# Kernel optimization log

Hardware: AMD Instinct MI355X
Metric: run time of the kernel (lower is better)

The kernel has to match this reference:

```python
import jax, jax.numpy as jnp
import numpy as np
from jax import lax

D_MODEL, D_STATE, D_CONV, EXPAND = 64, 16, 4, 2
D_INNER = EXPAND * D_MODEL          # 128
DT_RANK = (D_MODEL + 15) // 16      # 4 = ceil(d_model/16), mamba_ssm 'auto'
B, L, N_IDX = 512, 256, 2048


def setup_inputs() -> dict:
    key = jax.random.key(0)
    ks = jax.random.split(key, 14)
    g = lambda k, shape, s: jax.random.normal(k, shape, jnp.float32) * s
    return {
        "reads": jax.random.normal(ks[0], (B, L, 4), jnp.float32),
        "sequenced_reads_indices": jax.random.randint(ks[1], (N_IDX,), 0, B),
        "exp_w": g(ks[2], (4, D_MODEL), 0.5),
        "exp_b": jnp.zeros((D_MODEL,), jnp.float32),
        "in_proj_w": g(ks[3], (D_MODEL, 2 * D_INNER), 0.1),
        "conv_w": g(ks[4], (D_INNER, 1, D_CONV), 0.3),
        "conv_b": jnp.zeros((D_INNER,), jnp.float32),
        "x_proj_w": g(ks[5], (D_INNER, DT_RANK + 2 * D_STATE), 0.1),
        "dt_w": g(ks[6], (DT_RANK, D_INNER), 0.3),
        "dt_b": jnp.full((D_INNER,), -4.6, jnp.float32),  # softplus(-4.6) ~ 0.01, mamba dt init scale
        "A_log": jnp.log(jnp.broadcast_to(jnp.arange(1, D_STATE + 1, dtype=jnp.float32), (D_INNER, D_STATE))),
        "D_skip": jnp.ones((D_INNER,), jnp.float32),
        "out_proj_w": g(ks[7], (D_INNER, D_MODEL), 0.1),
        "q_w": g(ks[8], (2 * D_MODEL, D_MODEL), 0.1),
        "q_b": jnp.zeros((D_MODEL,), jnp.float32),
        "k_w": g(ks[9], (2 * D_MODEL, D_MODEL), 0.1),
        "k_b": jnp.zeros((D_MODEL,), jnp.float32),
    }


def _mamba(x, in_proj_w, conv_w, conv_b, x_proj_w, dt_w, dt_b, A_log, D_skip, out_proj_w):
    # x: [b, l, d_model]
    xm, z = jnp.split(x @ in_proj_w, 2, axis=-1)  # each [b, l, d_inner]
    # causal depthwise conv over the sequence axis (pad left by d_conv-1, truncate to l)
    xc = lax.conv_general_dilated(
        xm.transpose(0, 2, 1), conv_w, (1,), [(D_CONV - 1, 0)],
        dimension_numbers=("NCH", "OIH", "NCH"), feature_group_count=D_INNER)
    xc = jax.nn.silu(xc + conv_b[None, :, None]).transpose(0, 2, 1)  # [b, l, d_inner]
    dt, Bm, Cm = jnp.split(xc @ x_proj_w, [DT_RANK, DT_RANK + D_STATE], axis=-1)
    delta = jax.nn.softplus(dt @ dt_w + dt_b)  # [b, l, d_inner]
    A = -jnp.exp(A_log)                        # [d_inner, d_state]

    def step(h, inp):
        d_t, B_t, C_t, u_t = inp  # [b,di], [b,ds], [b,ds], [b,di]
        h = jnp.exp(d_t[:, :, None] * A) * h + (d_t * u_t)[:, :, None] * B_t[:, None, :]
        return h, jnp.einsum("bdn,bn->bd", h, C_t)

    h0 = jnp.zeros((x.shape[0], D_INNER, D_STATE), x.dtype)
    xs = (delta.transpose(1, 0, 2), Bm.transpose(1, 0, 2),
          Cm.transpose(1, 0, 2), xc.transpose(1, 0, 2))
    _, ys = lax.scan(jax.checkpoint(step), h0, xs)  # ys: [l, b, d_inner]
    y = ys.transpose(1, 0, 2) + xc * D_skip
    return (y * jax.nn.silu(z)) @ out_proj_w  # [b, l, d_model]


def reference(reads, sequenced_reads_indices, exp_w, exp_b, in_proj_w, conv_w, conv_b,
              x_proj_w, dt_w, dt_b, A_log, D_skip, out_proj_w, q_w, q_b, k_w, k_b):
    x = reads @ exp_w + exp_b  # [b, l, d_model]
    enc = _mamba(x, in_proj_w, conv_w, conv_b, x_proj_w, dt_w, dt_b, A_log, D_skip, out_proj_w)
    mean_pooled = enc.mean(axis=1)        # [b, d_model]
    last_pooled = enc[:, -1, :]           # [b, d_model] (max pool computed in torch but unused)
    pooled = jnp.concatenate([mean_pooled, last_pooled], axis=-1)  # [b, 2*d_model]
    seq = pooled[sequenced_reads_indices]  # [n, 2*d_model]
    queries = seq @ q_w + q_b
    keys = pooled @ k_w + k_b
    return jnp.einsum("nd,md->nm", queries, keys)  # [n, b]
```

## Files before the change

kernel.cpp:

```cpp
#include <hip/hip_runtime.h>
#include <math.h>

#define L_SEQ 256
#define TILE 16
#define NSEG 16

typedef __attribute__((ext_vector_type(2))) float f32x2;
typedef __attribute__((ext_vector_type(4))) float f32x4;
typedef __attribute__((ext_vector_type(8))) _Float16 f16x8;
typedef __attribute__((ext_vector_type(4))) _Float16 f16x4;
typedef __attribute__((ext_vector_type(2))) _Float16 f16x2;

__device__ __forceinline__ f32x2 fma2(f32x2 a, f32x2 b, f32x2 c) {
    return __builtin_elementwise_fma(a, b, c);
}
__device__ __forceinline__ f32x2 splat2(float x) { f32x2 v = {x, x}; return v; }
__device__ __forceinline__ float rcp_f(float x) {
#if __has_builtin(__builtin_amdgcn_rcpf)
    return __builtin_amdgcn_rcpf(x);
#else
    return 1.f / x;
#endif
}
__device__ __forceinline__ float silu_f(float x) { return x * rcp_f(1.f + __expf(-x)); }

__global__ __launch_bounds__(256)
void k_prep(const float* __restrict__ exp_w, const float* __restrict__ exp_b,
            const float* __restrict__ in_proj_w, const float* __restrict__ x_proj_w,
            const float* __restrict__ dt_w,
            const float* __restrict__ conv_w, const float* __restrict__ conv_b,
            const float* __restrict__ A_log,
            _Float16* __restrict__ WT, _Float16* __restrict__ W2,
            float* __restrict__ bias2, int* __restrict__ sflag)
{
    const int t = threadIdx.x, blk = blockIdx.x;
    if (blk < 5) {
        const int base = blk * 4096;
        for (int i = base + t; i < base + 4096; i += 256) {
            const int row = i >> 7, k = i & 127;
            float v;
            if (row < 128) {
                v = x_proj_w[k * 36 + 0] * dt_w[row]
                  + x_proj_w[k * 36 + 1] * dt_w[128 + row]
                  + x_proj_w[k * 36 + 2] * dt_w[256 + row]
                  + x_proj_w[k * 36 + 3] * dt_w[384 + row];
            } else {
                v = x_proj_w[k * 36 + 4 + (row - 128)];
            }
            WT[i] = (_Float16)v;
        }
    } else if (blk == 5) {
        const int d = t & 127;
        const int col = (t < 128) ? d : (128 + d);
        float w0 = 0, w1 = 0, w2 = 0, w3 = 0, bb = 0;
        for (int k = 0; k < 64; ++k) {
            float w = in_proj_w[k * 256 + col];
            w0 = fmaf(exp_w[k], w, w0);
            w1 = fmaf(exp_w[64 + k], w, w1);
            w2 = fmaf(exp_w[128 + k], w, w2);
            w3 = fmaf(exp_w[192 + k], w, w3);
            bb = fmaf(exp_b[k], w, bb);
        }
        const float wx[4] = {w0, w1, w2, w3};
        if (t < 128) {
            for (int j = 0; j < 32; ++j) {
                float v = 0.f;
                if (j < 16)      v = conv_w[d * 4 + (j >> 2)] * wx[j & 3];
                else if (j < 20) v = conv_w[d * 4 + (j - 16)] * bb;
                W2[d * 32 + j] = (_Float16)v;
            }
            bias2[d] = conv_b[d];
        } else {
            for (int j = 0; j < 32; ++j) {
                float v = 0.f;
                if (j >= 12 && j < 16) v = wx[j - 12];
                else if (j == 19)      v = bb;
                W2[(128 + d) * 32 + j] = (_Float16)v;
            }
        }
    } else {
        __shared__ int ok;
        if (t == 0) ok = 1;
        __syncthreads();
        bool good = true;
        for (int i = t; i < 2048; i += 256) {
            float a = -__expf(A_log[i]);
            good = good && (fabsf(a + (float)((i & 15) + 1)) < 1e-3f);
        }
        if (!good) atomicAnd(&ok, 0);
        __syncthreads();
        if (t == 0) sflag[0] = ok;
    }
}

__global__ __launch_bounds__(256, 8)
void mamba_seg(const float* __restrict__ reads,
               const _Float16* __restrict__ WT, const _Float16* __restrict__ W2,
               const float* __restrict__ bias2, const float* __restrict__ dt_b,
               const float* __restrict__ A_log, const float* __restrict__ D_skip,
               const int* __restrict__ sflag,
               f16x2* __restrict__ Qg, f16x2* __restrict__ Pg, f16x2* __restrict__ Kg,
               float* __restrict__ GS, float* __restrict__ CZ, float* __restrict__ SL,
               int Bn)
{
    const int bx = blockIdx.x;
    const int b = bx >> 4, sidx = bx & 15;
    const int l_off = sidx * TILE;
    const int t = threadIdx.x;
    const int dd = t >> 1, g = t & 1;

    __shared__ __align__(16) _Float16 F[TILE * 40];
    __shared__ __align__(16) _Float16 XC[TILE * 136];
    __shared__ __align__(8)  f16x2    DR[TILE * 130];
    __shared__ _Float16               ZS[TILE * 132];
    __shared__ __align__(16) float    BC[TILE * 32];

    const float dskip = D_skip[dd];
    const bool structured = (sflag[0] != 0);

    for (int i = t; i < TILE * 40; i += 256) {
        const int l = i / 40, j = i - l * 40;
        _Float16 v = (_Float16)0.f;
        if (j < 16) {
            const int row = l_off + l - 3 + (j >> 2);
            if (row >= 0) v = (_Float16)reads[((size_t)b * L_SEQ + row) * 4 + (j & 3)];
        } else if (j < 20) {
            v = (l_off + l - 3 + (j - 16) >= 0) ? (_Float16)1.f : (_Float16)0.f;
        }
        F[i] = v;
    }
    __syncthreads();

    const int lane = t & 63, wv = t >> 6;
    const int fcol = lane & 15, kq = lane >> 4, rbase = kq * 4;

#pragma unroll
    for (int i = 0; i < 4; ++i) {
        const int n = wv + 4 * i;
        f16x8 af = *(const f16x8*)&F[fcol * 40 + kq * 8];
        f16x8 bf = *(const f16x8*)&W2[(n * 16 + fcol) * 32 + kq * 8];
        f32x4 acc = {0.f, 0.f, 0.f, 0.f};
        acc = __builtin_amdgcn_mfma_f32_16x16x32_f16(af, bf, acc, 0, 0, 0);
        if (n < 8) {
            const int ch = n * 16 + fcol;
            const float bv = bias2[ch];
#pragma unroll
            for (int r = 0; r < 4; ++r)
                XC[(rbase + r) * 136 + ch] = (_Float16)silu_f(acc[r] + bv);
        } else {
            const int ch = (n - 8) * 16 + fcol;
#pragma unroll
            for (int r = 0; r < 4; ++r)
                ZS[(rbase + r) * 132 + ch] = (_Float16)silu_f(acc[r]);
        }
    }
    __syncthreads();

#pragma unroll
    for (int i = 0; i < 3; ++i) {
        const int n = wv + 4 * i;
        if (n < 10) {
            f32x4 acc = {0.f, 0.f, 0.f, 0.f};
#pragma unroll
            for (int ks = 0; ks < 4; ++ks) {
                const int ko = ks * 32 + kq * 8;
                f16x8 xa = *(const f16x8*)&XC[fcol * 136 + ko];
                f16x8 bf = *(const f16x8*)&WT[(n * 16 + fcol) * 128 + ko];
                acc = __builtin_amdgcn_mfma_f32_16x16x32_f16(xa, bf, acc, 0, 0, 0);
            }
            if (n < 8) {
                const int ch = n * 16 + fcol;
                const float db = dt_b[ch];
#pragma unroll
                for (int r = 0; r < 4; ++r) {
                    const float dtr = fminf(acc[r] + db, 80.f);
                    const float ex = __expf(dtr);
                    const float opx = 1.f + ex;
                    const float de = __logf(opx);
                    const float rr = rcp_f(opx);
                    DR[(rbase + r) * 130 + ch] = (f16x2){(_Float16)de, (_Float16)rr};
                }
            } else {
                const int jb = (n - 8) * 16 + fcol;
#pragma unroll
                for (int r = 0; r < 4; ++r)
                    BC[(rbase + r) * 32 + jb] = acc[r];
            }
        }
    }
    __syncthreads();

    f32x2 h2[4], P2[4], K2[4];
#pragma unroll
    for (int k = 0; k < 4; ++k) { h2[k] = splat2(0.f); P2[k] = splat2(1.f); K2[k] = splat2(0.f); }
    f32x2 gs2 = splat2(0.f);
    float xz = 0.f;
    {
        auto scan_loop = [&](bool needpk) {
            for (int l = 0; l < TILE; ++l) {
                const f16x2 dz = DR[l * 130 + dd];
                const float de = (float)dz[0];
                const float rr = (float)dz[1];
                const float zs = (float)ZS[l * 132 + dd];
                const float xc = (float)XC[l * 136 + dd];
                const float du = de * xc;
                f32x2 E2[4];
                if (structured) {
                    const float r2 = rr * rr;
                    const float r4 = r2 * r2;
                    const float t1 = g ? (r4 * r4 * rr) : rr;
                    E2[0] = (f32x2){t1, t1 * rr};
                    const f32x2 r2s = splat2(r2);
                    E2[1] = E2[0] * r2s;
                    E2[2] = E2[1] * r2s;
                    E2[3] = E2[2] * r2s;
                } else {
#pragma unroll
                    for (int k = 0; k < 4; ++k) {
                        float e0 = exp2f(de * (-__expf(A_log[dd * 16 + g * 8 + 2 * k])) * 1.44269504f);
                        float e1 = exp2f(de * (-__expf(A_log[dd * 16 + g * 8 + 2 * k + 1])) * 1.44269504f);
                        E2[k] = (f32x2){e0, e1};
                    }
                }
                const float4 Bq0 = *(const float4*)&BC[l * 32 + g * 8];
                const float4 Bq1 = *(const float4*)&BC[l * 32 + g * 8 + 4];
                const float4 Cq0 = *(const float4*)&BC[l * 32 + 16 + g * 8];
                const float4 Cq1 = *(const float4*)&BC[l * 32 + 16 + g * 8 + 4];
                const f32x2 B2[4] = {{Bq0.x, Bq0.y}, {Bq0.z, Bq0.w}, {Bq1.x, Bq1.y}, {Bq1.z, Bq1.w}};
                const f32x2 C2[4] = {{Cq0.x, Cq0.y}, {Cq0.z, Cq0.w}, {Cq1.x, Cq1.y}, {Cq1.z, Cq1.w}};
                const f32x2 dus = splat2(du), zss = splat2(zs);
                f32x2 yp2 = splat2(0.f);
#pragma unroll
                for (int k = 0; k < 4; ++k) {
                    h2[k] = fma2(E2[k], h2[k], dus * B2[k]);
                    yp2 = fma2(h2[k], C2[k], yp2);
                    if (needpk) {
                        P2[k] = P2[k] * E2[k];
                        K2[k] = fma2(zss, C2[k] * P2[k], K2[k]);
                    }
                }
                gs2 = fma2(yp2, zss, gs2);
                xz = fmaf(xc, zs, xz);
            }
        };
        if (sidx == 0) scan_loop(false);
        else           scan_loop(true);
    }

    {
        const size_t sb = (size_t)sidx * Bn + b;
#pragma unroll
        for (int k = 0; k < 4; ++k) {
            const size_t o = (sb * 8 + g * 4 + k) * 128 + dd;
            Qg[o] = (f16x2){(_Float16)h2[k].x, (_Float16)h2[k].y};
            if (sidx != 0) {
                Pg[o] = (f16x2){(_Float16)P2[k].x, (_Float16)P2[k].y};
                Kg[o] = (f16x2){(_Float16)K2[k].x, (_Float16)K2[k].y};
            }
        }
        float gsp = gs2.x + gs2.y;
        gsp += __shfl_xor(gsp, 1);
        const float gsum = fmaf(dskip, xz, gsp);
        if (g == 0) GS[sb * 128 + dd] = gsum;
        if (sidx == NSEG - 1) {
            const float zs_last = (float)ZS[(TILE - 1) * 132 + dd];
            const float xc_last = (float)XC[(TILE - 1) * 136 + dd];
#pragma unroll
            for (int k = 0; k < 8; ++k)
                CZ[((size_t)b * 16 + g * 8 + k) * 128 + dd] =
                    zs_last * BC[(TILE - 1) * 32 + 16 + g * 8 + k];
            if (g == 0) SL[(size_t)b * 128 + dd] = zs_last * xc_last * dskip;
        }
    }
}

template<int NS>
__global__ __launch_bounds__(256)
void stitch(const f16x2* __restrict__ Qg, const f16x2* __restrict__ Pg,
            const f16x2* __restrict__ Kg, const float* __restrict__ GS,
            const float* __restrict__ CZ, const float* __restrict__ SL,
            const float* __restrict__ out_proj_w,
            const float* __restrict__ k_w, const float* __restrict__ k_b,
            float* __restrict__ pooled, float* __restrict__ keysT, int Bn)
{
    const int b = blockIdx.x, t = threadIdx.x;
    const int d = t >> 1, g = t & 1;
    __shared__ float gb[256];
    __shared__ float pl[128];

    float h[8];
    float gsum = (g == 0) ? GS[(size_t)b * 128 + d] : 0.f;
#pragma unroll
    for (int k = 0; k < 4; ++k) {
        f16x2 q = Qg[((size_t)b * 8 + g * 4 + k) * 128 + d];
        h[2 * k] = (float)q[0]; h[2 * k + 1] = (float)q[1];
    }
#pragma unroll
    for (int s = 1; s < NS; ++s) {
        const size_t sb = (size_t)s * Bn + b;
        if (g == 0) gsum += GS[sb * 128 + d];
        float corr = 0.f;
#pragma unroll
        for (int k = 0; k < 4; ++k) {
            const size_t o = (sb * 8 + g * 4 + k) * 128 + d;
            f16x2 qv = Qg[o], pv = Pg[o], kv = Kg[o];
            corr = fmaf((float)kv[0], h[2 * k], corr);
            corr = fmaf((float)kv[1], h[2 * k + 1], corr);
            h[2 * k]     = fmaf((float)pv[0], h[2 * k],     (float)qv[0]);
            h[2 * k + 1] = fmaf((float)pv[1], h[2 * k + 1], (float)qv[1]);
        }
        gsum += corr;
    }
    float glast = (g == 0) ? SL[(size_t)b * 128 + d] : 0.f;
#pragma unroll
    for (int k = 0; k < 8; ++k)
        glast = fmaf(CZ[((size_t)b * 16 + g * 8 + k) * 128 + d], h[k], glast);

    gsum += __shfl_xor(gsum, 1);
    glast += __shfl_xor(glast, 1);
    if (g == 0) { gb[d] = gsum * (1.f / (float)L_SEQ); gb[128 + d] = glast; }
    __syncthreads();

    {
        const int oi = t >> 1;
        const int half = oi >> 6, oc = oi & 63;
        const float* gbp = &gb[half * 128];
        float s = 0.f;
#pragma unroll 16
        for (int i = g * 64; i < g * 64 + 64; ++i)
            s = fmaf(gbp[i], out_proj_w[i * 64 + oc], s);
        s += __shfl_xor(s, 1);
        if (g == 0) { pooled[(size_t)b * 128 + oi] = s; pl[oi] = s; }
    }
    __syncthreads();

    if (t < 128) {
        const int oc = t >> 1;
        float s = (g == 0) ? k_b[oc] : 0.f;
#pragma unroll 16
        for (int i = g * 64; i < g * 64 + 64; ++i)
            s = fmaf(pl[i], k_w[i * 64 + oc], s);
        s += __shfl_xor(s, 1);
        if (g == 0) keysT[(size_t)oc * Bn + b] = s;
    }
}

__global__ __launch_bounds__(128)
void qk_kernel(const float* __restrict__ pooled, const int* __restrict__ idx,
               const float* __restrict__ q_w, const float* __restrict__ q_b,
               const float* __restrict__ keysT, float* __restrict__ out, int B, int N)
{
    const int n0 = blockIdx.x * 2, t = threadIdx.x;
    const int n1 = n0 + 1;
    const bool has1 = (n1 < N);
    __shared__ float p0[128], p1[128];
    __shared__ float q0[64], q1[64];
    const int bi0 = idx[n0];
    const int bi1 = has1 ? idx[n1] : bi0;
    p0[t] = pooled[(size_t)bi0 * 128 + t];
    p1[t] = pooled[(size_t)bi1 * 128 + t];
    __syncthreads();
    if (t < 64) {
        float s = q_b[t];
#pragma unroll
        for (int i = 0; i < 128; ++i) s = fmaf(p0[i], q_w[i * 64 + t], s);
        q0[t] = s;
    } else {
        const int tt = t - 64;
        float s = q_b[tt];
#pragma unroll
        for (int i = 0; i < 128; ++i) s = fmaf(p1[i], q_w[i * 64 + tt], s);
        q1[tt] = s;
    }
    __syncthreads();
    for (int m0 = t * 4; m0 < B; m0 += 512) {
        f32x4 a0 = {0.f, 0.f, 0.f, 0.f}, a1 = {0.f, 0.f, 0.f, 0.f};
#pragma unroll 8
        for (int i = 0; i < 64; ++i) {
            const float4 kv = *(const float4*)&keysT[(size_t)i * B + m0];
            const float qa = q0[i], qb = q1[i];
            a0[0] = fmaf(qa, kv.x, a0[0]); a0[1] = fmaf(qa, kv.y, a0[1]);
            a0[2] = fmaf(qa, kv.z, a0[2]); a0[3] = fmaf(qa, kv.w, a0[3]);
            a1[0] = fmaf(qb, kv.x, a1[0]); a1[1] = fmaf(qb, kv.y, a1[1]);
            a1[2] = fmaf(qb, kv.z, a1[2]); a1[3] = fmaf(qb, kv.w, a1[3]);
        }
        *(f32x4*)&out[(size_t)n0 * B + m0] = a0;
        if (has1) *(f32x4*)&out[(size_t)n1 * B + m0] = a1;
    }
}


extern "C" void kernel_launch(void* const* d_in, const int* in_sizes, int n_in,
                              void* d_out, int out_size, void* d_ws, size_t ws_size,
                              hipStream_t stream)
{
    const float* reads      = (const float*)d_in[0];
    const int*   idx        = (const int*)d_in[1];
    const float* exp_w      = (const float*)d_in[2];
    const float* exp_b      = (const float*)d_in[3];
    const float* in_proj_w  = (const float*)d_in[4];
    const float* conv_w     = (const float*)d_in[5];
    const float* conv_b     = (const float*)d_in[6];
    const float* x_proj_w   = (const float*)d_in[7];
    const float* dt_w       = (const float*)d_in[8];
    const float* dt_b       = (const float*)d_in[9];
    const float* A_log      = (const float*)d_in[10];
    const float* D_skip     = (const float*)d_in[11];
    const float* out_proj_w = (const float*)d_in[12];
    const float* q_w        = (const float*)d_in[13];
    const float* q_b        = (const float*)d_in[14];
    const float* k_w        = (const float*)d_in[15];
    const float* k_b        = (const float*)d_in[16];

    const int B = in_sizes[0] / (L_SEQ * 4);
    const int N = in_sizes[1];

    char* wsb = (char*)d_ws;
    size_t off = 0;
    auto alloc = [&](size_t bytes) {
        size_t o = off;
        off = (off + bytes + 255) & ~(size_t)255;
        return o;
    };

    float*     pooled = (float*)(wsb + alloc((size_t)B * 128 * 4));
    float*     keysT  = (float*)(wsb + alloc((size_t)B * 64 * 4));
    _Float16*  WT     = (_Float16*)(wsb + alloc(160 * 128 * 2));
    _Float16*  W2     = (_Float16*)(wsb + alloc(256 * 32 * 2));
    float*     bias2  = (float*)(wsb + alloc(128 * 4));
    int*       sflag  = (int*)(wsb + alloc(256));

    const size_t pairs = (size_t)B * NSEG * 8 * 128;
    f16x2* Qg = (f16x2*)(wsb + alloc(pairs * 4));
    f16x2* Pg = (f16x2*)(wsb + alloc(pairs * 4));
    f16x2* Kg = (f16x2*)(wsb + alloc(pairs * 4));
    float* GS = (float*)(wsb + alloc((size_t)B * NSEG * 128 * 4));
    float* CZ = (float*)(wsb + alloc((size_t)B * 16 * 128 * 4));
    float* SL = (float*)(wsb + alloc((size_t)B * 128 * 4));

    k_prep<<<7, 256, 0, stream>>>(exp_w, exp_b, in_proj_w, x_proj_w, dt_w,
                                  conv_w, conv_b, A_log, WT, W2, bias2, sflag);
    mamba_seg<<<B * NSEG, 256, 0, stream>>>(reads, WT, W2, bias2, dt_b,
                                            A_log, D_skip, sflag, Qg, Pg, Kg,
                                            GS, CZ, SL, B);
    stitch<NSEG><<<B, 256, 0, stream>>>(Qg, Pg, Kg, GS, CZ, SL, out_proj_w, k_w, k_b,
                                        pooled, keysT, B);
    qk_kernel<<<(N + 1) / 2, 128, 0, stream>>>(pooled, idx, q_w, q_b, keysT,
                                               (float*)d_out, B, N);
}
```

Baseline: 125.9 us.

## Vectorize segment-state stores and reconstruct decay products from a scalar ratio

Segment-boundary states Q and K are now packed as one 16-byte f16x8 per thread instead of four f16x2 writes, so each thread issues a single wide store and the stitch kernel a single wide load. When A has the structured -(n+1) pattern, the per-state decay products P are not stored. Only the base ratio R is written, and stitch rebuilds P as successive powers of R. This cuts global write and read traffic between the two kernels, at the cost of a few extra multiplies and a branch on the structure flag in stitch.

Result: faster. 121.6 us (-3.5%).

```diff
diff --git a/kernel.cpp b/kernel.cpp
--- a/kernel.cpp
+++ b/kernel.cpp
@@ -99,7 +99,8 @@
                const float* __restrict__ bias2, const float* __restrict__ dt_b,
                const float* __restrict__ A_log, const float* __restrict__ D_skip,
                const int* __restrict__ sflag,
-               f16x2* __restrict__ Qg, f16x2* __restrict__ Pg, f16x2* __restrict__ Kg,
+               f16x8* __restrict__ Qg8, f16x8* __restrict__ Pg8, f16x8* __restrict__ Kg8,
+               float* __restrict__ Rg,
                float* __restrict__ GS, float* __restrict__ CZ, float* __restrict__ SL,
                int Bn)
 {
@@ -249,13 +250,32 @@
 
     {
         const size_t sb = (size_t)sidx * Bn + b;
+        const size_t rowq = (sb * 2 + g) * 128 + dd;
+        f16x8 qv;
 #pragma unroll
         for (int k = 0; k < 4; ++k) {
-            const size_t o = (sb * 8 + g * 4 + k) * 128 + dd;
-            Qg[o] = (f16x2){(_Float16)h2[k].x, (_Float16)h2[k].y};
-            if (sidx != 0) {
-                Pg[o] = (f16x2){(_Float16)P2[k].x, (_Float16)P2[k].y};
-                Kg[o] = (f16x2){(_Float16)K2[k].x, (_Float16)K2[k].y};
+            qv[2 * k]     = (_Float16)h2[k].x;
+            qv[2 * k + 1] = (_Float16)h2[k].y;
+        }
+        Qg8[rowq] = qv;
+        if (sidx != 0) {
+            f16x8 kv;
+#pragma unroll
+            for (int k = 0; k < 4; ++k) {
+                kv[2 * k]     = (_Float16)K2[k].x;
+                kv[2 * k + 1] = (_Float16)K2[k].y;
+            }
+            Kg8[rowq] = kv;
+            if (structured) {
+                if (g == 0) Rg[sb * 128 + dd] = P2[0].x;
+            } else {
+                f16x8 pv;
+#pragma unroll
+                for (int k = 0; k < 4; ++k) {
+                    pv[2 * k]     = (_Float16)P2[k].x;
+                    pv[2 * k + 1] = (_Float16)P2[k].y;
+                }
+                Pg8[rowq] = pv;
             }
         }
         float gsp = gs2.x + gs2.y;
@@ -276,38 +296,54 @@
 
 template<int NS>
 __global__ __launch_bounds__(256)
-void stitch(const f16x2* __restrict__ Qg, const f16x2* __restrict__ Pg,
-            const f16x2* __restrict__ Kg, const float* __restrict__ GS,
+void stitch(const f16x8* __restrict__ Qg8, const f16x8* __restrict__ Pg8,
+            const f16x8* __restrict__ Kg8, const float* __restrict__ Rg,
+            const float* __restrict__ GS,
             const float* __restrict__ CZ, const float* __restrict__ SL,
+            const int* __restrict__ sflag,
             const float* __restrict__ out_proj_w,
             const float* __restrict__ k_w, const float* __restrict__ k_b,
             float* __restrict__ pooled, float* __restrict__ keysT, int Bn)
 {
     const int b = blockIdx.x, t = threadIdx.x;
     const int d = t >> 1, g = t & 1;
+    const bool structured = (sflag[0] != 0);
     __shared__ float gb[256];
     __shared__ float pl[128];
 
     float h[8];
     float gsum = (g == 0) ? GS[(size_t)b * 128 + d] : 0.f;
-#pragma unroll
-    for (int k = 0; k < 4; ++k) {
-        f16x2 q = Qg[((size_t)b * 8 + g * 4 + k) * 128 + d];
-        h[2 * k] = (float)q[0]; h[2 * k + 1] = (float)q[1];
+    {
+        f16x8 qv = Qg8[((size_t)b * 2 + g) * 128 + d];
+#pragma unroll
+        for (int j = 0; j < 8; ++j) h[j] = (float)qv[j];
     }
 #pragma unroll
     for (int s = 1; s < NS; ++s) {
         const size_t sb = (size_t)s * Bn + b;
         if (g == 0) gsum += GS[sb * 128 + d];
+        const size_t rowq = (sb * 2 + g) * 128 + d;
+        const f16x8 qv = Qg8[rowq];
+        const f16x8 kv = Kg8[rowq];
+        float P[8];
+        if (structured) {
+            const float R = Rg[sb * 128 + d];
+            const float R2 = R * R;
+            float t1 = R;
+            if (g) { const float R4 = R2 * R2; t1 = R4 * R4 * R; }
+            P[0] = t1;
+#pragma unroll
+            for (int j = 1; j < 8; ++j) P[j] = P[j - 1] * R;
+        } else {
+            const f16x8 pv = Pg8[rowq];
+#pragma unroll
+            for (int j = 0; j < 8; ++j) P[j] = (float)pv[j];
+        }
         float corr = 0.f;
 #pragma unroll
-        for (int k = 0; k < 4; ++k) {
-            const size_t o = (sb * 8 + g * 4 + k) * 128 + d;
-            f16x2 qv = Qg[o], pv = Pg[o], kv = Kg[o];
-            corr = fmaf((float)kv[0], h[2 * k], corr);
-            corr = fmaf((float)kv[1], h[2 * k + 1], corr);
-            h[2 * k]     = fmaf((float)pv[0], h[2 * k],     (float)qv[0]);
-            h[2 * k + 1] = fmaf((float)pv[1], h[2 * k + 1], (float)qv[1]);
+        for (int j = 0; j < 8; ++j) {
+            corr = fmaf((float)kv[j], h[j], corr);
+            h[j] = fmaf(P[j], h[j], (float)qv[j]);
         }
         gsum += corr;
     }
@@ -430,21 +466,23 @@
     float*     bias2  = (float*)(wsb + alloc(128 * 4));
     int*       sflag  = (int*)(wsb + alloc(256));
 
-    const size_t pairs = (size_t)B * NSEG * 8 * 128;
-    f16x2* Qg = (f16x2*)(wsb + alloc(pairs * 4));
-    f16x2* Pg = (f16x2*)(wsb + alloc(pairs * 4));
-    f16x2* Kg = (f16x2*)(wsb + alloc(pairs * 4));
-    float* GS = (float*)(wsb + alloc((size_t)B * NSEG * 128 * 4));
-    float* CZ = (float*)(wsb + alloc((size_t)B * 16 * 128 * 4));
-    float* SL = (float*)(wsb + alloc((size_t)B * 128 * 4));
+    const size_t rows8 = (size_t)B * NSEG * 2 * 128;
+    f16x8* Qg8 = (f16x8*)(wsb + alloc(rows8 * 16));
+    f16x8* Kg8 = (f16x8*)(wsb + alloc(rows8 * 16));
+    f16x8* Pg8 = (f16x8*)(wsb + alloc(rows8 * 16));
+    float* Rg  = (float*)Pg8;
+    float* GS  = (float*)(wsb + alloc((size_t)B * NSEG * 128 * 4));
+    float* CZ  = (float*)(wsb + alloc((size_t)B * 16 * 128 * 4));
+    float* SL  = (float*)(wsb + alloc((size_t)B * 128 * 4));
 
     k_prep<<<7, 256, 0, stream>>>(exp_w, exp_b, in_proj_w, x_proj_w, dt_w,
                                   conv_w, conv_b, A_log, WT, W2, bias2, sflag);
     mamba_seg<<<B * NSEG, 256, 0, stream>>>(reads, WT, W2, bias2, dt_b,
-                                            A_log, D_skip, sflag, Qg, Pg, Kg,
+                                            A_log, D_skip, sflag,
+                                            Qg8, Pg8, Kg8, Rg,
                                             GS, CZ, SL, B);
-    stitch<NSEG><<<B, 256, 0, stream>>>(Qg, Pg, Kg, GS, CZ, SL, out_proj_w, k_w, k_b,
-                                        pooled, keysT, B);
+    stitch<NSEG><<<B, 256, 0, stream>>>(Qg8, Pg8, Kg8, Rg, GS, CZ, SL, sflag,
+                                        out_proj_w, k_w, k_b, pooled, keysT, B);
     qk_kernel<<<(N + 1) / 2, 128, 0, stream>>>(pooled, idx, q_w, q_b, keysT,
                                                (float*)d_out, B, N);
 }
```
